# Performance work log

Hardware: AMD Instinct MI355X
Metric: run time of the kernel (lower is better)

## Reference

```python
import jax, jax.numpy as jnp
import numpy as np

N = 100000

def gcn_conv(x, src, dst, norm, W, b, num_nodes):
    # x: [N, Cin] -> [N, Cout]; GCNConv: linear transform then normalized sum aggregation
    h = x @ W                                   # [N, Cout]
    msg = h[src] * norm[:, None]                # [E+N, Cout] gather + scale
    out = jax.ops.segment_sum(msg, dst, num_segments=num_nodes)  # scatter-add
    return out + b

def _norm_coeffs(src, dst, num_nodes):
    # symmetric normalization D^{-1/2} A_hat D^{-1/2} with self-loops already in src/dst
    deg = jax.ops.segment_sum(jnp.ones_like(src, dtype=jnp.float32), dst, num_segments=num_nodes)
    dinv = jnp.where(deg > 0, jax.lax.rsqrt(jnp.maximum(deg, 1.0)), 0.0)
    return dinv[src] * dinv[dst]

def setup_inputs() -> dict:
    key = jax.random.key(0)
    ks = jax.random.split(key, 8)
    Cin, Ch, Cout, E = 128, 128, 47, 1600000
    x = jax.random.normal(ks[0], (N, Cin), dtype=jnp.float32)
    edge_index = jax.random.randint(ks[1], (2, E), 0, N, dtype=jnp.int64)
    def glorot(k, fan_in, fan_out):
        s = jnp.sqrt(6.0 / (fan_in + fan_out))
        return jax.random.uniform(k, (fan_in, fan_out), jnp.float32, -s, s)
    return {
        'x': x, 'edge_index': edge_index,
        'W1': glorot(ks[2], Cin, Ch), 'b1': jnp.zeros((Ch,), jnp.float32),
        'W2': glorot(ks[3], Ch, Ch),  'b2': jnp.zeros((Ch,), jnp.float32),
        'W3': glorot(ks[4], Ch, Cout),'b3': jnp.zeros((Cout,), jnp.float32),
    }

def reference(x, edge_index, W1, b1, W2, b2, W3, b3):
    num_nodes = x.shape[0]
    loop = jnp.arange(num_nodes, dtype=edge_index.dtype)
    src = jnp.concatenate([edge_index[0], loop])
    dst = jnp.concatenate([edge_index[1], loop])
    norm = _norm_coeffs(src, dst, num_nodes)
    # eval-mode forward: dropout(p=0.5, training=False) is identity
    h = gcn_conv(x, src, dst, norm, W1, b1, num_nodes)
    h = jax.nn.relu(h)
    h = gcn_conv(h, src, dst, norm, W2, b2, num_nodes)
    h = jax.nn.relu(h)
    h = gcn_conv(h, src, dst, norm, W3, b3, num_nodes)
    return jax.nn.log_softmax(h, axis=1)
```

## Files before the change

kernel.cpp:

```cpp
#include <hip/hip_runtime.h>
#include <stdint.h>

typedef __bf16 bf16x8 __attribute__((ext_vector_type(8)));
typedef float f32x4 __attribute__((ext_vector_type(4)));

#define CHB 8192

__device__ __forceinline__ float bf2f(unsigned short s) {
    union { unsigned u; float f; } x; x.u = ((unsigned)s) << 16; return x.f;
}
__device__ __forceinline__ float bitf(unsigned u) {
    union { unsigned u; float f; } x; x.u = u; return x.f;
}
__device__ __forceinline__ unsigned short f2bf(float f) {
    union { float f; unsigned u; } x; x.f = f;
    unsigned r = x.u + 0x7fffu + ((x.u >> 16) & 1u);
    return (unsigned short)(r >> 16);
}

__device__ __forceinline__ void dot2acc(float& a, unsigned pk, unsigned sel) {
    asm("v_dot2_f32_bf16 %0, %1, %2, %0" : "+v"(a) : "v"(pk), "v"(sel));
}

__global__ __launch_bounds__(256) void k_hist(const int* __restrict__ dst, int E, int nPB,
                                              int* __restrict__ bhist, int NB) {
    __shared__ int h[256];
    int t = threadIdx.x;
    h[t] = 0;
    __syncthreads();
    int blk = blockIdx.x;
    int hi = min((blk + 1) * CHB, E);
    for (int e = blk * CHB + t; e < hi; e += 256) atomicAdd(&h[dst[e] >> 9], 1);
    __syncthreads();
    if (t < NB) bhist[t * nPB + blk] = h[t];
}

__global__ __launch_bounds__(256) void k_scan_part(const int* __restrict__ deg,
                                                   int* __restrict__ part, int N) {
    __shared__ int wsum[4];
    int t = threadIdx.x;
    int lane = t & 63, wv = t >> 6;
    int base = blockIdx.x * 1024 + t * 4;
    int s = 0;
#pragma unroll
    for (int j = 0; j < 4; ++j) {
        int i = base + j;
        if (i < N) s += deg[i];
    }
    for (int off = 1; off < 64; off <<= 1) s += __shfl_xor(s, off, 64);
    if (lane == 0) wsum[wv] = s;
    __syncthreads();
    if (t == 0) part[blockIdx.x] = wsum[0] + wsum[1] + wsum[2] + wsum[3];
}

__global__ void k_scan_mid(int* __restrict__ part, int nb) {
    __shared__ int buf[256];
    int t = threadIdx.x;
    buf[t] = (t < nb) ? part[t] : 0;
    __syncthreads();
    for (int off = 1; off < 256; off <<= 1) {
        int v = buf[t];
        int u = (t >= off) ? buf[t - off] : 0;
        __syncthreads();
        buf[t] = v + u;
        __syncthreads();
    }
    if (t < nb) part[t] = (t == 0) ? 0 : buf[t - 1];
}

__global__ __launch_bounds__(256) void k_scan_final(const int* __restrict__ deg,
                                                    const int* __restrict__ part,
                                                    int* __restrict__ out, int N) {
    __shared__ int wsum[4];
    int t = threadIdx.x;
    int lane = t & 63, wv = t >> 6;
    int base = blockIdx.x * 1024 + t * 4;
    int v[4];
    int s = 0;
#pragma unroll
    for (int j = 0; j < 4; ++j) {
        int i = base + j;
        v[j] = (i < N) ? deg[i] : 0;
        s += v[j];
    }
    int inc = s;
    for (int off = 1; off < 64; off <<= 1) {
        int u = __shfl_up(inc, off, 64);
        if (lane >= off) inc += u;
    }
    if (lane == 63) wsum[wv] = inc;
    __syncthreads();
    int excl = part[blockIdx.x] + inc - s;
    for (int w = 0; w < wv; ++w) excl += wsum[w];
#pragma unroll
    for (int j = 0; j < 4; ++j) {
        int i = base + j;
        if (i < N) {
            out[i] = excl;
            excl += v[j];
            if (i == N - 1) out[N] = excl;
        }
    }
}

__global__ __launch_bounds__(256) void k_partition(const int* __restrict__ src,
                                                   const int* __restrict__ dst, int E,
                                                   int nPB, const int* __restrict__ bscan,
                                                   unsigned* __restrict__ part_edges, int NB) {
    __shared__ int cur[256];
    int t = threadIdx.x;
    int blk = blockIdx.x;
    if (t < NB) cur[t] = bscan[t * nPB + blk];
    __syncthreads();
    int hi = min((blk + 1) * CHB, E);
    for (int e = blk * CHB + t; e < hi; e += 256) {
        int d = dst[e];
        int s = src[e];
        int pos = atomicAdd(&cur[d >> 9], 1);
        part_edges[pos] = ((unsigned)(d & 511) << 17) | (unsigned)s;
    }
}

__global__ __launch_bounds__(256) void k_bucket(const unsigned* __restrict__ part_edges,
                                                const int* __restrict__ bscan, int nPB,
                                                int N, int Npad, int* __restrict__ row_ptr,
                                                float* __restrict__ dinv,
                                                int* __restrict__ ssrc) {
    __shared__ int cnt[512];
    __shared__ int excl[512];
    __shared__ int wsum[4];
    int t = threadIdx.x;
    int b = blockIdx.x;
    int pb = bscan[b * nPB];
    int pe = bscan[(b + 1) * nPB];
    cnt[t] = 0; cnt[t + 256] = 0;
    __syncthreads();
    for (int e = pb + t; e < pe; e += 256)
        atomicAdd(&cnt[(part_edges[e] >> 17) & 511], 1);
    __syncthreads();
    int a0 = cnt[2 * t], a1 = cnt[2 * t + 1];
    int s = a0 + a1;
    int lane = t & 63, wv = t >> 6;
    int inc = s;
    for (int off = 1; off < 64; off <<= 1) {
        int u = __shfl_up(inc, off, 64);
        if (lane >= off) inc += u;
    }
    if (lane == 63) wsum[wv] = inc;
    __syncthreads();
    int pre = inc - s;
    for (int w = 0; w < wv; ++w) pre += wsum[w];
    excl[2 * t] = pre;
    excl[2 * t + 1] = pre + a0;
    int base = b << 9;
#pragma unroll
    for (int j = 0; j < 2; ++j) {
        int i = 2 * t + j;
        int g = base + i;
        int c = (j == 0) ? a0 : a1;
        int ex = (j == 0) ? pre : pre + a0;
        if (g < N) {
            row_ptr[g] = pb + ex;
            if (g == N - 1) row_ptr[N] = pb + ex + c;
        }
        if (g < Npad) dinv[g] = rsqrtf((float)c + 1.0f);
    }
    __syncthreads();
    for (int e = pb + t; e < pe; e += 256) {
        unsigned pk = part_edges[e];
        int doff = (pk >> 17) & 511;
        int pos = pb + atomicAdd(&excl[doff], 1);
        ssrc[pos] = (int)(pk & 0x1FFFFu);
    }
}

__global__ void k_cvt_x(const float4* __restrict__ x, ushort4* __restrict__ out, int n4) {
    int i = blockIdx.x * blockDim.x + threadIdx.x;
    if (i < n4) {
        float4 v = x[i];
        ushort4 o;
        o.x = f2bf(v.x); o.y = f2bf(v.y); o.z = f2bf(v.z); o.w = f2bf(v.w);
        out[i] = o;
    }
}

__global__ void k_wfrag(const float* __restrict__ W, unsigned short* __restrict__ Wf,
                        int Ncol, int realCols) {
    int NT = Ncol >> 4;
    int total = 4 * NT * 64 * 8;
    int idx = blockIdx.x * blockDim.x + threadIdx.x;
    if (idx >= total) return;
    int j = idx & 7;
    int l = (idx >> 3) & 63;
    int t = idx >> 9;
    int n = t % NT;
    int kk = t / NT;
    int k = kk * 32 + ((l >> 4) << 3) + j;
    int c = (n << 4) + (l & 15);
    float v = (c < realCols) ? W[k * realCols + c] : 0.0f;
    Wf[idx] = f2bf(v);
}

template<int NT>
__global__ __launch_bounds__(256) void k_gemm(const unsigned short* __restrict__ A,
                                              const unsigned short* __restrict__ Wf,
                                              const float* __restrict__ dinv,
                                              unsigned short* __restrict__ Hout) {
    int lane = threadIdx.x & 63;
    int wv = threadIdx.x >> 6;
    int rb = blockIdx.x * 4 + wv;
    size_t row0 = (size_t)rb * 16;
    const unsigned short* arow = A + (row0 + (lane & 15)) * 128 + ((lane >> 4) << 3);
    f32x4 acc[NT];
#pragma unroll
    for (int n = 0; n < NT; ++n) acc[n] = (f32x4){0.f, 0.f, 0.f, 0.f};
#pragma unroll
    for (int kk = 0; kk < 4; ++kk) {
        bf16x8 a = *(const bf16x8*)(arow + kk * 32);
#pragma unroll
        for (int n = 0; n < NT; ++n) {
            bf16x8 b = *(const bf16x8*)(Wf + (((kk * NT + n) * 64 + lane) << 3));
            acc[n] = __builtin_amdgcn_mfma_f32_16x16x32_bf16(a, b, acc[n], 0, 0, 0);
        }
    }
    const int NCOL = NT * 16;
    size_t crow = row0 + ((lane >> 4) << 2);
    int ccol = lane & 15;
    float dv[4];
#pragma unroll
    for (int q = 0; q < 4; ++q) dv[q] = dinv[crow + q];
#pragma unroll
    for (int n = 0; n < NT; ++n) {
#pragma unroll
        for (int q = 0; q < 4; ++q) {
            Hout[(crow + q) * NCOL + n * 16 + ccol] = f2bf(acc[n][q] * dv[q]);
        }
    }
}

#define SEL_LO 0x00003F80u
#define SEL_HI 0x3F800000u

#define DOT8(v)                                      \
    dot2acc(acc[0], (v).x, sel_lo); dot2acc(acc[1], (v).x, sel_hi); \
    dot2acc(acc[2], (v).y, sel_lo); dot2acc(acc[3], (v).y, sel_hi); \
    dot2acc(acc[4], (v).z, sel_lo); dot2acc(acc[5], (v).z, sel_hi); \
    dot2acc(acc[6], (v).w, sel_lo); dot2acc(acc[7], (v).w, sel_hi);

#define DOT4(v)                                      \
    dot2acc(acc[0], (v).x, sel_lo); dot2acc(acc[1], (v).x, sel_hi); \
    dot2acc(acc[2], (v).y, sel_lo); dot2acc(acc[3], (v).y, sel_hi);

__global__ __launch_bounds__(256) void k_agg(const unsigned short* __restrict__ H,
                                             const int* __restrict__ row_ptr,
                                             const int* __restrict__ ssrc,
                                             const float* __restrict__ dinv,
                                             const float* __restrict__ bias,
                                             unsigned short* __restrict__ Out, int N) {
    int lane = threadIdx.x & 63;
    int i = blockIdx.x * 4 + (threadIdx.x >> 6);
    if (i >= N) return;
    unsigned sel_lo = SEL_LO, sel_hi = SEL_HI;
    int g = lane >> 4;
    int c16 = lane & 15;
    const uint4* Hv = (const uint4*)H;
    float acc[8];
#pragma unroll
    for (int c = 0; c < 8; ++c) acc[c] = 0.f;
    int e0 = row_ptr[i], e1 = row_ptr[i + 1];
    for (int base = e0; base < e1; base += 64) {
        int cnt = min(64, e1 - base);
        int sidx = (lane < cnt) ? ssrc[base + lane] : 0;
        int full = cnt & ~3;
#pragma unroll 4
        for (int j = 0; j < full; j += 4) {
            int s = __shfl(sidx, j + g, 64);
            uint4 v = Hv[((size_t)s << 4) + c16];
            DOT8(v);
        }
        int jj = full + g;
        if (jj < cnt) {
            int s = __shfl(sidx, jj, 64);
            uint4 v = Hv[((size_t)s << 4) + c16];
            DOT8(v);
        }
    }
    if (g == 0) {
        uint4 v = Hv[((size_t)i << 4) + c16];
        DOT8(v);
    }
#pragma unroll
    for (int c = 0; c < 8; ++c) {
        acc[c] += __shfl_xor(acc[c], 16, 64);
        acc[c] += __shfl_xor(acc[c], 32, 64);
    }
    if (g == 0) {
        float dv = dinv[i];
        const float4* bv = (const float4*)bias;
        float4 b0 = bv[c16 * 2], b1 = bv[c16 * 2 + 1];
        float r0 = fmaxf(acc[0] * dv + b0.x, 0.f);
        float r1 = fmaxf(acc[1] * dv + b0.y, 0.f);
        float r2 = fmaxf(acc[2] * dv + b0.z, 0.f);
        float r3 = fmaxf(acc[3] * dv + b0.w, 0.f);
        float r4 = fmaxf(acc[4] * dv + b1.x, 0.f);
        float r5 = fmaxf(acc[5] * dv + b1.y, 0.f);
        float r6 = fmaxf(acc[6] * dv + b1.z, 0.f);
        float r7 = fmaxf(acc[7] * dv + b1.w, 0.f);
        uint4 o;
        o.x = (unsigned)f2bf(r0) | ((unsigned)f2bf(r1) << 16);
        o.y = (unsigned)f2bf(r2) | ((unsigned)f2bf(r3) << 16);
        o.z = (unsigned)f2bf(r4) | ((unsigned)f2bf(r5) << 16);
        o.w = (unsigned)f2bf(r6) | ((unsigned)f2bf(r7) << 16);
        ((uint4*)Out)[((size_t)i << 4) + c16] = o;
    }
}

__global__ __launch_bounds__(256) void k_agg3(const unsigned short* __restrict__ H,
                                              const int* __restrict__ row_ptr,
                                              const int* __restrict__ ssrc,
                                              const float* __restrict__ dinv,
                                              const float* __restrict__ b3,
                                              float* __restrict__ Out, int N, int Cout) {
    int lane = threadIdx.x & 63;
    int i = blockIdx.x * 4 + (threadIdx.x >> 6);
    if (i >= N) return;
    unsigned sel_lo = SEL_LO, sel_hi = SEL_HI;
    int g = lane >> 4;
    int c16 = lane & 15;
    const uint2* Hv = (const uint2*)H;
    float acc[4];
#pragma unroll
    for (int c = 0; c < 4; ++c) acc[c] = 0.f;
    int e0 = row_ptr[i], e1 = row_ptr[i + 1];
    for (int base = e0; base < e1; base += 64) {
        int cnt = min(64, e1 - base);
        int sidx = (lane < cnt) ? ssrc[base + lane] : 0;
        int full = cnt & ~3;
#pragma unroll 4
        for (int j = 0; j < full; j += 4) {
            int s = __shfl(sidx, j + g, 64);
            uint2 v = Hv[((size_t)s << 4) + c16];
            DOT4(v);
        }
        int jj = full + g;
        if (jj < cnt) {
            int s = __shfl(sidx, jj, 64);
            uint2 v = Hv[((size_t)s << 4) + c16];
            DOT4(v);
        }
    }
    if (g == 0) {
        uint2 v = Hv[((size_t)i << 4) + c16];
        DOT4(v);
    }
#pragma unroll
    for (int c = 0; c < 4; ++c) {
        acc[c] += __shfl_xor(acc[c], 16, 64);
        acc[c] += __shfl_xor(acc[c], 32, 64);
    }
    float t0 = __shfl(acc[0], lane >> 2, 64);
    float t1 = __shfl(acc[1], lane >> 2, 64);
    float t2 = __shfl(acc[2], lane >> 2, 64);
    float t3 = __shfl(acc[3], lane >> 2, 64);
    float a01 = (lane & 1) ? t1 : t0;
    float a23 = (lane & 1) ? t3 : t2;
    float av  = (lane & 2) ? a23 : a01;
    float dv = dinv[i];
    float z = (lane < Cout) ? av * dv + b3[lane] : -1e30f;
    float m = z;
    for (int off = 32; off; off >>= 1) m = fmaxf(m, __shfl_xor(m, off, 64));
    float pexp = (lane < Cout) ? expf(z - m) : 0.f;
    float ssum = pexp;
    for (int off = 32; off; off >>= 1) ssum += __shfl_xor(ssum, off, 64);
    if (lane < Cout) Out[(size_t)i * Cout + lane] = z - m - logf(ssum);
}

extern "C" void kernel_launch(void* const* d_in, const int* in_sizes, int n_in,
                              void* d_out, int out_size, void* d_ws, size_t ws_size,
                              hipStream_t stream) {
    const float* x  = (const float*)d_in[0];
    const int*   ei = (const int*)d_in[1];
    const float* W1 = (const float*)d_in[2];
    const float* b1 = (const float*)d_in[3];
    const float* W2 = (const float*)d_in[4];
    const float* b2 = (const float*)d_in[5];
    const float* W3 = (const float*)d_in[6];
    const float* b3 = (const float*)d_in[7];

    const int N = in_sizes[0] / 128;
    const int E = in_sizes[1] / 2;
    const int Cout = in_sizes[7];
    const int Npad = (N + 63) & ~63;
    const int* srcp = ei;
    const int* dstp = ei + E;

    const int NB  = (N + 511) >> 9;
    const int nPB = (E + CHB - 1) / CHB;
    const int M   = NB * nPB;

    char* p = (char*)d_ws;
    auto alloc = [&](size_t bytes) -> void* {
        void* r = (void*)p;
        p += (bytes + 255) & ~(size_t)255;
        return r;
    };
    float* dinv     = (float*)alloc((size_t)Npad * 4);
    int*   row_ptr  = (int*)alloc((size_t)(N + 1) * 4);
    int*   bhist    = (int*)alloc((size_t)M * 4);
    int*   bscan    = (int*)alloc((size_t)(M + 1) * 4);
    int*   part     = (int*)alloc(1024 * 4);
    unsigned* pedge = (unsigned*)alloc((size_t)E * 4);
    int*   ssrc     = (int*)alloc((size_t)E * 4);
    unsigned short* xb  = (unsigned short*)alloc((size_t)Npad * 128 * 2);
    unsigned short* hb  = (unsigned short*)alloc((size_t)Npad * 128 * 2);
    unsigned short* ab  = (unsigned short*)alloc((size_t)Npad * 128 * 2);
    unsigned short* wf1 = (unsigned short*)alloc(128 * 128 * 2);
    unsigned short* wf2 = (unsigned short*)alloc(128 * 128 * 2);
    unsigned short* wf3 = (unsigned short*)alloc(128 * 64 * 2);

    const int nb2 = (M + 1023) / 1024;
    k_hist<<<nPB, 256, 0, stream>>>(dstp, E, nPB, bhist, NB);
    k_scan_part<<<nb2, 256, 0, stream>>>(bhist, part, M);
    k_scan_mid<<<1, 256, 0, stream>>>(part, nb2);
    k_scan_final<<<nb2, 256, 0, stream>>>(bhist, part, bscan, M);
    k_partition<<<nPB, 256, 0, stream>>>(srcp, dstp, E, nPB, bscan, pedge, NB);
    k_bucket<<<NB, 256, 0, stream>>>(pedge, bscan, nPB, N, Npad, row_ptr, dinv, ssrc);

    k_cvt_x<<<(N * 128 / 4 + 255) / 256, 256, 0, stream>>>((const float4*)x, (ushort4*)xb,
                                                           N * 128 / 4);
    k_wfrag<<<(16384 + 255) / 256, 256, 0, stream>>>(W1, wf1, 128, 128);
    k_wfrag<<<(16384 + 255) / 256, 256, 0, stream>>>(W2, wf2, 128, 128);
    k_wfrag<<<(8192 + 255) / 256, 256, 0, stream>>>(W3, wf3, 64, Cout);

    const int gemmGrid = Npad / 64;
    const int aggGrid = (N + 3) / 4;

    k_gemm<8><<<gemmGrid, 256, 0, stream>>>(xb, wf1, dinv, hb);
    k_agg<<<aggGrid, 256, 0, stream>>>(hb, row_ptr, ssrc, dinv, b1, ab, N);
    k_gemm<8><<<gemmGrid, 256, 0, stream>>>(ab, wf2, dinv, hb);
    k_agg<<<aggGrid, 256, 0, stream>>>(hb, row_ptr, ssrc, dinv, b2, ab, N);
    k_gemm<4><<<gemmGrid, 256, 0, stream>>>(ab, wf3, dinv, hb);
    k_agg3<<<aggGrid, 256, 0, stream>>>(hb, row_ptr, ssrc, dinv, b3,
                                        (float*)d_out, N, Cout);
}
```

Baseline: 303.7 us.

## Map one node per 16-lane quarter-wave in aggregation kernels

The aggregation kernels now assign each node to a 16-lane group instead of a full 64-lane wave, so each wave processes four nodes and every block covers sixteen. Each group walks its own edge list serially, loading indices directly, which removes the cross-group shuffles and the final reduction across lanes. The log-softmax in the last layer becomes a 16-lane reduction over four channels per lane. In exchange, lanes within a wave can diverge when neighbouring nodes have different degrees, and per-edge index loads are no longer coalesced.

```diff
diff --git a/kernel.cpp b/kernel.cpp
--- a/kernel.cpp
+++ b/kernel.cpp
@@ -8,9 +8,6 @@
 
 __device__ __forceinline__ float bf2f(unsigned short s) {
     union { unsigned u; float f; } x; x.u = ((unsigned)s) << 16; return x.f;
-}
-__device__ __forceinline__ float bitf(unsigned u) {
-    union { unsigned u; float f; } x; x.u = u; return x.f;
 }
 __device__ __forceinline__ unsigned short f2bf(float f) {
     union { float f; unsigned u; } x; x.f = f;
@@ -258,61 +255,43 @@
                                              const float* __restrict__ bias,
                                              unsigned short* __restrict__ Out, int N) {
     int lane = threadIdx.x & 63;
-    int i = blockIdx.x * 4 + (threadIdx.x >> 6);
+    int g = lane >> 4;
+    int c16 = lane & 15;
+    int i = blockIdx.x * 16 + ((threadIdx.x >> 6) << 2) + g;
     if (i >= N) return;
     unsigned sel_lo = SEL_LO, sel_hi = SEL_HI;
-    int g = lane >> 4;
-    int c16 = lane & 15;
     const uint4* Hv = (const uint4*)H;
     float acc[8];
 #pragma unroll
     for (int c = 0; c < 8; ++c) acc[c] = 0.f;
-    int e0 = row_ptr[i], e1 = row_ptr[i + 1];
-    for (int base = e0; base < e1; base += 64) {
-        int cnt = min(64, e1 - base);
-        int sidx = (lane < cnt) ? ssrc[base + lane] : 0;
-        int full = cnt & ~3;
-#pragma unroll 4
-        for (int j = 0; j < full; j += 4) {
-            int s = __shfl(sidx, j + g, 64);
-            uint4 v = Hv[((size_t)s << 4) + c16];
-            DOT8(v);
-        }
-        int jj = full + g;
-        if (jj < cnt) {
-            int s = __shfl(sidx, jj, 64);
-            uint4 v = Hv[((size_t)s << 4) + c16];
-            DOT8(v);
-        }
-    }
-    if (g == 0) {
+    {
         uint4 v = Hv[((size_t)i << 4) + c16];
         DOT8(v);
     }
-#pragma unroll
-    for (int c = 0; c < 8; ++c) {
-        acc[c] += __shfl_xor(acc[c], 16, 64);
-        acc[c] += __shfl_xor(acc[c], 32, 64);
-    }
-    if (g == 0) {
-        float dv = dinv[i];
-        const float4* bv = (const float4*)bias;
-        float4 b0 = bv[c16 * 2], b1 = bv[c16 * 2 + 1];
-        float r0 = fmaxf(acc[0] * dv + b0.x, 0.f);
-        float r1 = fmaxf(acc[1] * dv + b0.y, 0.f);
-        float r2 = fmaxf(acc[2] * dv + b0.z, 0.f);
-        float r3 = fmaxf(acc[3] * dv + b0.w, 0.f);
-        float r4 = fmaxf(acc[4] * dv + b1.x, 0.f);
-        float r5 = fmaxf(acc[5] * dv + b1.y, 0.f);
-        float r6 = fmaxf(acc[6] * dv + b1.z, 0.f);
-        float r7 = fmaxf(acc[7] * dv + b1.w, 0.f);
-        uint4 o;
-        o.x = (unsigned)f2bf(r0) | ((unsigned)f2bf(r1) << 16);
-        o.y = (unsigned)f2bf(r2) | ((unsigned)f2bf(r3) << 16);
-        o.z = (unsigned)f2bf(r4) | ((unsigned)f2bf(r5) << 16);
-        o.w = (unsigned)f2bf(r6) | ((unsigned)f2bf(r7) << 16);
-        ((uint4*)Out)[((size_t)i << 4) + c16] = o;
-    }
+    int e0 = row_ptr[i], e1 = row_ptr[i + 1];
+#pragma unroll 2
+    for (int e = e0; e < e1; ++e) {
+        int s = ssrc[e];
+        uint4 v = Hv[((size_t)s << 4) + c16];
+        DOT8(v);
+    }
+    float dv = dinv[i];
+    const float4* bv = (const float4*)bias;
+    float4 b0 = bv[c16 * 2], b1 = bv[c16 * 2 + 1];
+    float r0 = fmaxf(acc[0] * dv + b0.x, 0.f);
+    float r1 = fmaxf(acc[1] * dv + b0.y, 0.f);
+    float r2 = fmaxf(acc[2] * dv + b0.z, 0.f);
+    float r3 = fmaxf(acc[3] * dv + b0.w, 0.f);
+    float r4 = fmaxf(acc[4] * dv + b1.x, 0.f);
+    float r5 = fmaxf(acc[5] * dv + b1.y, 0.f);
+    float r6 = fmaxf(acc[6] * dv + b1.z, 0.f);
+    float r7 = fmaxf(acc[7] * dv + b1.w, 0.f);
+    uint4 o;
+    o.x = (unsigned)f2bf(r0) | ((unsigned)f2bf(r1) << 16);
+    o.y = (unsigned)f2bf(r2) | ((unsigned)f2bf(r3) << 16);
+    o.z = (unsigned)f2bf(r4) | ((unsigned)f2bf(r5) << 16);
+    o.w = (unsigned)f2bf(r6) | ((unsigned)f2bf(r7) << 16);
+    ((uint4*)Out)[((size_t)i << 4) + c16] = o;
 }
 
 __global__ __launch_bounds__(256) void k_agg3(const unsigned short* __restrict__ H,
@@ -322,57 +301,51 @@
                                               const float* __restrict__ b3,
                                               float* __restrict__ Out, int N, int Cout) {
     int lane = threadIdx.x & 63;
-    int i = blockIdx.x * 4 + (threadIdx.x >> 6);
+    int g = lane >> 4;
+    int c16 = lane & 15;
+    int i = blockIdx.x * 16 + ((threadIdx.x >> 6) << 2) + g;
     if (i >= N) return;
     unsigned sel_lo = SEL_LO, sel_hi = SEL_HI;
-    int g = lane >> 4;
-    int c16 = lane & 15;
     const uint2* Hv = (const uint2*)H;
     float acc[4];
 #pragma unroll
     for (int c = 0; c < 4; ++c) acc[c] = 0.f;
-    int e0 = row_ptr[i], e1 = row_ptr[i + 1];
-    for (int base = e0; base < e1; base += 64) {
-        int cnt = min(64, e1 - base);
-        int sidx = (lane < cnt) ? ssrc[base + lane] : 0;
-        int full = cnt & ~3;
-#pragma unroll 4
-        for (int j = 0; j < full; j += 4) {
-            int s = __shfl(sidx, j + g, 64);
-            uint2 v = Hv[((size_t)s << 4) + c16];
-            DOT4(v);
-        }
-        int jj = full + g;
-        if (jj < cnt) {
-            int s = __shfl(sidx, jj, 64);
-            uint2 v = Hv[((size_t)s << 4) + c16];
-            DOT4(v);
-        }
-    }
-    if (g == 0) {
+    {
         uint2 v = Hv[((size_t)i << 4) + c16];
         DOT4(v);
     }
+    int e0 = row_ptr[i], e1 = row_ptr[i + 1];
+#pragma unroll 2
+    for (int e = e0; e < e1; ++e) {
+        int s = ssrc[e];
+        uint2 v = Hv[((size_t)s << 4) + c16];
+        DOT4(v);
+    }
+    float dv = dinv[i];
+    float z[4];
+    float m = -1e30f;
 #pragma unroll
     for (int c = 0; c < 4; ++c) {
-        acc[c] += __shfl_xor(acc[c], 16, 64);
-        acc[c] += __shfl_xor(acc[c], 32, 64);
-    }
-    float t0 = __shfl(acc[0], lane >> 2, 64);
-    float t1 = __shfl(acc[1], lane >> 2, 64);
-    float t2 = __shfl(acc[2], lane >> 2, 64);
-    float t3 = __shfl(acc[3], lane >> 2, 64);
-    float a01 = (lane & 1) ? t1 : t0;
-    float a23 = (lane & 1) ? t3 : t2;
-    float av  = (lane & 2) ? a23 : a01;
-    float dv = dinv[i];
-    float z = (lane < Cout) ? av * dv + b3[lane] : -1e30f;
-    float m = z;
-    for (int off = 32; off; off >>= 1) m = fmaxf(m, __shfl_xor(m, off, 64));
-    float pexp = (lane < Cout) ? expf(z - m) : 0.f;
-    float ssum = pexp;
-    for (int off = 32; off; off >>= 1) ssum += __shfl_xor(ssum, off, 64);
-    if (lane < Cout) Out[(size_t)i * Cout + lane] = z - m - logf(ssum);
+        int ch = c16 * 4 + c;
+        z[c] = (ch < Cout) ? acc[c] * dv + b3[ch] : -1e30f;
+        m = fmaxf(m, z[c]);
+    }
+#pragma unroll
+    for (int off = 1; off < 16; off <<= 1) m = fmaxf(m, __shfl_xor(m, off, 64));
+    float ssum = 0.f;
+#pragma unroll
+    for (int c = 0; c < 4; ++c) {
+        int ch = c16 * 4 + c;
+        if (ch < Cout) ssum += expf(z[c] - m);
+    }
+#pragma unroll
+    for (int off = 1; off < 16; off <<= 1) ssum += __shfl_xor(ssum, off, 64);
+    float lg = m + logf(ssum);
+#pragma unroll
+    for (int c = 0; c < 4; ++c) {
+        int ch = c16 * 4 + c;
+        if (ch < Cout) Out[(size_t)i * Cout + ch] = z[c] - lg;
+    }
 }
 
 extern "C" void kernel_launch(void* const* d_in, const int* in_sizes, int n_in,
@@ -433,7 +406,7 @@
     k_wfrag<<<(8192 + 255) / 256, 256, 0, stream>>>(W3, wf3, 64, Cout);
 
     const int gemmGrid = Npad / 64;
-    const int aggGrid = (N + 3) / 4;
+    const int aggGrid = (N + 15) / 16;
 
     k_gemm<8><<<gemmGrid, 256, 0, stream>>>(xb, wf1, dinv, hb);
     k_agg<<<aggGrid, 256, 0, stream>>>(hb, row_ptr, ssrc, dinv, b1, ab, N);
```

New measurement: 322.1 us. 6.0% more time.

## Fuse aggregation with next-layer GEMM via LDS and fold x conversion into GEMM

Applied to the files above, without the earlier changes.

The first GEMM now reads fp32 x directly and converts to bf16 in registers, so the separate conversion kernel and its bf16 buffer go away. Each aggregation for layers 1 and 2 is fused with the following layer's MFMA GEMM. A block aggregates 64 nodes into an LDS tile, then multiplies that tile by the next weight matrix, which removes a full write and re-read of the intermediate activation. In exchange, each wave walks 16 nodes one after another, and there are far fewer blocks. That cuts the parallelism available to hide the latency of the irregular gathers and can leave load imbalance across waves.

```diff
diff --git a/kernel.cpp b/kernel.cpp
--- a/kernel.cpp
+++ b/kernel.cpp
@@ -5,13 +5,8 @@
 typedef float f32x4 __attribute__((ext_vector_type(4)));
 
 #define CHB 8192
-
-__device__ __forceinline__ float bf2f(unsigned short s) {
-    union { unsigned u; float f; } x; x.u = ((unsigned)s) << 16; return x.f;
-}
-__device__ __forceinline__ float bitf(unsigned u) {
-    union { unsigned u; float f; } x; x.u = u; return x.f;
-}
+#define LDSROW 17
+
 __device__ __forceinline__ unsigned short f2bf(float f) {
     union { float f; unsigned u; } x; x.f = f;
     unsigned r = x.u + 0x7fffu + ((x.u >> 16) & 1u);
@@ -21,6 +16,19 @@
 __device__ __forceinline__ void dot2acc(float& a, unsigned pk, unsigned sel) {
     asm("v_dot2_f32_bf16 %0, %1, %2, %0" : "+v"(a) : "v"(pk), "v"(sel));
 }
+
+#define SEL_LO 0x00003F80u
+#define SEL_HI 0x3F800000u
+
+#define DOT8(v)                                      \
+    dot2acc(acc[0], (v).x, sel_lo); dot2acc(acc[1], (v).x, sel_hi); \
+    dot2acc(acc[2], (v).y, sel_lo); dot2acc(acc[3], (v).y, sel_hi); \
+    dot2acc(acc[4], (v).z, sel_lo); dot2acc(acc[5], (v).z, sel_hi); \
+    dot2acc(acc[6], (v).w, sel_lo); dot2acc(acc[7], (v).w, sel_hi);
+
+#define DOT4(v)                                      \
+    dot2acc(acc[0], (v).x, sel_lo); dot2acc(acc[1], (v).x, sel_hi); \
+    dot2acc(acc[2], (v).y, sel_lo); dot2acc(acc[3], (v).y, sel_hi);
 
 __global__ __launch_bounds__(256) void k_hist(const int* __restrict__ dst, int E, int nPB,
                                               int* __restrict__ bhist, int NB) {
@@ -171,16 +179,6 @@
         int doff = (pk >> 17) & 511;
         int pos = pb + atomicAdd(&excl[doff], 1);
         ssrc[pos] = (int)(pk & 0x1FFFFu);
-    }
-}
-
-__global__ void k_cvt_x(const float4* __restrict__ x, ushort4* __restrict__ out, int n4) {
-    int i = blockIdx.x * blockDim.x + threadIdx.x;
-    if (i < n4) {
-        float4 v = x[i];
-        ushort4 o;
-        o.x = f2bf(v.x); o.y = f2bf(v.y); o.z = f2bf(v.z); o.w = f2bf(v.w);
-        out[i] = o;
     }
 }
 
@@ -201,117 +199,153 @@
     Wf[idx] = f2bf(v);
 }
 
-template<int NT>
-__global__ __launch_bounds__(256) void k_gemm(const unsigned short* __restrict__ A,
-                                              const unsigned short* __restrict__ Wf,
-                                              const float* __restrict__ dinv,
-                                              unsigned short* __restrict__ Hout) {
+__global__ __launch_bounds__(256) void k_gemm_f32(const float* __restrict__ X,
+                                                  const unsigned short* __restrict__ Wf,
+                                                  const float* __restrict__ dinv,
+                                                  unsigned short* __restrict__ Hout, int N) {
     int lane = threadIdx.x & 63;
     int wv = threadIdx.x >> 6;
-    int rb = blockIdx.x * 4 + wv;
-    size_t row0 = (size_t)rb * 16;
-    const unsigned short* arow = A + (row0 + (lane & 15)) * 128 + ((lane >> 4) << 3);
-    f32x4 acc[NT];
-#pragma unroll
-    for (int n = 0; n < NT; ++n) acc[n] = (f32x4){0.f, 0.f, 0.f, 0.f};
+    size_t row0 = (size_t)(blockIdx.x * 4 + wv) * 16;
+    int arowi = (int)row0 + (lane & 15);
+    const float* arow = X + (size_t)arowi * 128 + ((lane >> 4) << 3);
+    bool vr = arowi < N;
+    f32x4 acc[8];
+#pragma unroll
+    for (int n = 0; n < 8; ++n) acc[n] = (f32x4){0.f, 0.f, 0.f, 0.f};
 #pragma unroll
     for (int kk = 0; kk < 4; ++kk) {
-        bf16x8 a = *(const bf16x8*)(arow + kk * 32);
-#pragma unroll
-        for (int n = 0; n < NT; ++n) {
-            bf16x8 b = *(const bf16x8*)(Wf + (((kk * NT + n) * 64 + lane) << 3));
-            acc[n] = __builtin_amdgcn_mfma_f32_16x16x32_bf16(a, b, acc[n], 0, 0, 0);
-        }
-    }
-    const int NCOL = NT * 16;
+        union { bf16x8 v; unsigned short u[8]; } A;
+        if (vr) {
+            float4 f0 = *(const float4*)(arow + kk * 32);
+            float4 f1 = *(const float4*)(arow + kk * 32 + 4);
+            A.u[0] = f2bf(f0.x); A.u[1] = f2bf(f0.y);
+            A.u[2] = f2bf(f0.z); A.u[3] = f2bf(f0.w);
+            A.u[4] = f2bf(f1.x); A.u[5] = f2bf(f1.y);
+            A.u[6] = f2bf(f1.z); A.u[7] = f2bf(f1.w);
+        } else {
+#pragma unroll
+            for (int j = 0; j < 8; ++j) A.u[j] = 0;
+        }
+#pragma unroll
+        for (int n = 0; n < 8; ++n) {
+            bf16x8 b = *(const bf16x8*)(Wf + (((kk * 8 + n) * 64 + lane) << 3));
+            acc[n] = __builtin_amdgcn_mfma_f32_16x16x32_bf16(A.v, b, acc[n], 0, 0, 0);
+        }
+    }
     size_t crow = row0 + ((lane >> 4) << 2);
     int ccol = lane & 15;
     float dv[4];
 #pragma unroll
     for (int q = 0; q < 4; ++q) dv[q] = dinv[crow + q];
 #pragma unroll
-    for (int n = 0; n < NT; ++n) {
+    for (int n = 0; n < 8; ++n) {
 #pragma unroll
         for (int q = 0; q < 4; ++q) {
-            Hout[(crow + q) * NCOL + n * 16 + ccol] = f2bf(acc[n][q] * dv[q]);
-        }
-    }
-}
-
-#define SEL_LO 0x00003F80u
-#define SEL_HI 0x3F800000u
-
-#define DOT8(v)                                      \
-    dot2acc(acc[0], (v).x, sel_lo); dot2acc(acc[1], (v).x, sel_hi); \
-    dot2acc(acc[2], (v).y, sel_lo); dot2acc(acc[3], (v).y, sel_hi); \
-    dot2acc(acc[4], (v).z, sel_lo); dot2acc(acc[5], (v).z, sel_hi); \
-    dot2acc(acc[6], (v).w, sel_lo); dot2acc(acc[7], (v).w, sel_hi);
-
-#define DOT4(v)                                      \
-    dot2acc(acc[0], (v).x, sel_lo); dot2acc(acc[1], (v).x, sel_hi); \
-    dot2acc(acc[2], (v).y, sel_lo); dot2acc(acc[3], (v).y, sel_hi);
-
-__global__ __launch_bounds__(256) void k_agg(const unsigned short* __restrict__ H,
-                                             const int* __restrict__ row_ptr,
-                                             const int* __restrict__ ssrc,
-                                             const float* __restrict__ dinv,
-                                             const float* __restrict__ bias,
-                                             unsigned short* __restrict__ Out, int N) {
+            Hout[(crow + q) * 128 + n * 16 + ccol] = f2bf(acc[n][q] * dv[q]);
+        }
+    }
+}
+
+template<int NT>
+__global__ __launch_bounds__(256) void k_agg_gemm(const unsigned short* __restrict__ H,
+                                                  const int* __restrict__ row_ptr,
+                                                  const int* __restrict__ ssrc,
+                                                  const float* __restrict__ dinv,
+                                                  const float* __restrict__ bias,
+                                                  const unsigned short* __restrict__ Wf,
+                                                  unsigned short* __restrict__ Hout, int N) {
+    __shared__ uint4 lds[64 * LDSROW];
     int lane = threadIdx.x & 63;
-    int i = blockIdx.x * 4 + (threadIdx.x >> 6);
-    if (i >= N) return;
-    unsigned sel_lo = SEL_LO, sel_hi = SEL_HI;
+    int wv = threadIdx.x >> 6;
     int g = lane >> 4;
     int c16 = lane & 15;
+    unsigned sel_lo = SEL_LO, sel_hi = SEL_HI;
     const uint4* Hv = (const uint4*)H;
-    float acc[8];
-#pragma unroll
-    for (int c = 0; c < 8; ++c) acc[c] = 0.f;
-    int e0 = row_ptr[i], e1 = row_ptr[i + 1];
-    for (int base = e0; base < e1; base += 64) {
-        int cnt = min(64, e1 - base);
-        int sidx = (lane < cnt) ? ssrc[base + lane] : 0;
-        int full = cnt & ~3;
+    const int iBase = blockIdx.x * 64 + wv * 16;
+
+    for (int ii = 0; ii < 16; ++ii) {
+        int i = iBase + ii;
+        float acc[8];
+#pragma unroll
+        for (int c = 0; c < 8; ++c) acc[c] = 0.f;
+        if (i < N) {
+            if (g == 0) {
+                uint4 v = Hv[((size_t)i << 4) + c16];
+                DOT8(v);
+            }
+            int e0 = row_ptr[i], e1 = row_ptr[i + 1];
+            for (int base = e0; base < e1; base += 64) {
+                int cnt = min(64, e1 - base);
+                int sidx = (lane < cnt) ? ssrc[base + lane] : 0;
+                int full = cnt & ~3;
 #pragma unroll 4
-        for (int j = 0; j < full; j += 4) {
-            int s = __shfl(sidx, j + g, 64);
-            uint4 v = Hv[((size_t)s << 4) + c16];
-            DOT8(v);
-        }
-        int jj = full + g;
-        if (jj < cnt) {
-            int s = __shfl(sidx, jj, 64);
-            uint4 v = Hv[((size_t)s << 4) + c16];
-            DOT8(v);
-        }
-    }
-    if (g == 0) {
-        uint4 v = Hv[((size_t)i << 4) + c16];
-        DOT8(v);
-    }
-#pragma unroll
-    for (int c = 0; c < 8; ++c) {
-        acc[c] += __shfl_xor(acc[c], 16, 64);
-        acc[c] += __shfl_xor(acc[c], 32, 64);
-    }
-    if (g == 0) {
-        float dv = dinv[i];
-        const float4* bv = (const float4*)bias;
-        float4 b0 = bv[c16 * 2], b1 = bv[c16 * 2 + 1];
-        float r0 = fmaxf(acc[0] * dv + b0.x, 0.f);
-        float r1 = fmaxf(acc[1] * dv + b0.y, 0.f);
-        float r2 = fmaxf(acc[2] * dv + b0.z, 0.f);
-        float r3 = fmaxf(acc[3] * dv + b0.w, 0.f);
-        float r4 = fmaxf(acc[4] * dv + b1.x, 0.f);
-        float r5 = fmaxf(acc[5] * dv + b1.y, 0.f);
-        float r6 = fmaxf(acc[6] * dv + b1.z, 0.f);
-        float r7 = fmaxf(acc[7] * dv + b1.w, 0.f);
-        uint4 o;
-        o.x = (unsigned)f2bf(r0) | ((unsigned)f2bf(r1) << 16);
-        o.y = (unsigned)f2bf(r2) | ((unsigned)f2bf(r3) << 16);
-        o.z = (unsigned)f2bf(r4) | ((unsigned)f2bf(r5) << 16);
-        o.w = (unsigned)f2bf(r6) | ((unsigned)f2bf(r7) << 16);
-        ((uint4*)Out)[((size_t)i << 4) + c16] = o;
+                for (int j = 0; j < full; j += 4) {
+                    int s = __shfl(sidx, j + g, 64);
+                    uint4 v = Hv[((size_t)s << 4) + c16];
+                    DOT8(v);
+                }
+                int jj = full + g;
+                if (jj < cnt) {
+                    int s = __shfl(sidx, jj, 64);
+                    uint4 v = Hv[((size_t)s << 4) + c16];
+                    DOT8(v);
+                }
+            }
+        }
+#pragma unroll
+        for (int c = 0; c < 8; ++c) {
+            acc[c] += __shfl_xor(acc[c], 16, 64);
+            acc[c] += __shfl_xor(acc[c], 32, 64);
+        }
+        if (g == 0) {
+            float dv = dinv[i];
+            const float4* bv = (const float4*)bias;
+            float4 b0 = bv[c16 * 2], b1 = bv[c16 * 2 + 1];
+            float r0 = fmaxf(acc[0] * dv + b0.x, 0.f);
+            float r1 = fmaxf(acc[1] * dv + b0.y, 0.f);
+            float r2 = fmaxf(acc[2] * dv + b0.z, 0.f);
+            float r3 = fmaxf(acc[3] * dv + b0.w, 0.f);
+            float r4 = fmaxf(acc[4] * dv + b1.x, 0.f);
+            float r5 = fmaxf(acc[5] * dv + b1.y, 0.f);
+            float r6 = fmaxf(acc[6] * dv + b1.z, 0.f);
+            float r7 = fmaxf(acc[7] * dv + b1.w, 0.f);
+            uint4 o;
+            o.x = (unsigned)f2bf(r0) | ((unsigned)f2bf(r1) << 16);
+            o.y = (unsigned)f2bf(r2) | ((unsigned)f2bf(r3) << 16);
+            o.z = (unsigned)f2bf(r4) | ((unsigned)f2bf(r5) << 16);
+            o.w = (unsigned)f2bf(r6) | ((unsigned)f2bf(r7) << 16);
+            lds[(wv * 16 + ii) * LDSROW + c16] = o;
+        }
+    }
+    __syncthreads();
+
+    f32x4 gacc[NT];
+#pragma unroll
+    for (int n = 0; n < NT; ++n) gacc[n] = (f32x4){0.f, 0.f, 0.f, 0.f};
+    const uint4* arow = &lds[(wv * 16 + (lane & 15)) * LDSROW];
+#pragma unroll
+    for (int kk = 0; kk < 4; ++kk) {
+        union { bf16x8 v; uint4 q; } A;
+        A.q = arow[kk * 4 + (lane >> 4)];
+#pragma unroll
+        for (int n = 0; n < NT; ++n) {
+            bf16x8 b = *(const bf16x8*)(Wf + (((kk * NT + n) * 64 + lane) << 3));
+            gacc[n] = __builtin_amdgcn_mfma_f32_16x16x32_bf16(A.v, b, gacc[n], 0, 0, 0);
+        }
+    }
+    const int NCOL = NT * 16;
+    size_t row0 = (size_t)iBase;
+    size_t crow = row0 + ((lane >> 4) << 2);
+    int ccol = lane & 15;
+    float dv[4];
+#pragma unroll
+    for (int q = 0; q < 4; ++q) dv[q] = dinv[crow + q];
+#pragma unroll
+    for (int n = 0; n < NT; ++n) {
+#pragma unroll
+        for (int q = 0; q < 4; ++q) {
+            Hout[(crow + q) * NCOL + n * 16 + ccol] = f2bf(gacc[n][q] * dv[q]);
+        }
     }
 }
 
@@ -411,7 +445,6 @@
     int*   part     = (int*)alloc(1024 * 4);
     unsigned* pedge = (unsigned*)alloc((size_t)E * 4);
     int*   ssrc     = (int*)alloc((size_t)E * 4);
-    unsigned short* xb  = (unsigned short*)alloc((size_t)Npad * 128 * 2);
     unsigned short* hb  = (unsigned short*)alloc((size_t)Npad * 128 * 2);
     unsigned short* ab  = (unsigned short*)alloc((size_t)Npad * 128 * 2);
     unsigned short* wf1 = (unsigned short*)alloc(128 * 128 * 2);
@@ -426,8 +459,6 @@
     k_partition<<<nPB, 256, 0, stream>>>(srcp, dstp, E, nPB, bscan, pedge, NB);
     k_bucket<<<NB, 256, 0, stream>>>(pedge, bscan, nPB, N, Npad, row_ptr, dinv, ssrc);
 
-    k_cvt_x<<<(N * 128 / 4 + 255) / 256, 256, 0, stream>>>((const float4*)x, (ushort4*)xb,
-                                                           N * 128 / 4);
     k_wfrag<<<(16384 + 255) / 256, 256, 0, stream>>>(W1, wf1, 128, 128);
     k_wfrag<<<(16384 + 255) / 256, 256, 0, stream>>>(W2, wf2, 128, 128);
     k_wfrag<<<(8192 + 255) / 256, 256, 0, stream>>>(W3, wf3, 64, Cout);
@@ -435,11 +466,9 @@
     const int gemmGrid = Npad / 64;
     const int aggGrid = (N + 3) / 4;
 
-    k_gemm<8><<<gemmGrid, 256, 0, stream>>>(xb, wf1, dinv, hb);
-    k_agg<<<aggGrid, 256, 0, stream>>>(hb, row_ptr, ssrc, dinv, b1, ab, N);
-    k_gemm<8><<<gemmGrid, 256, 0, stream>>>(ab, wf2, dinv, hb);
-    k_agg<<<aggGrid, 256, 0, stream>>>(hb, row_ptr, ssrc, dinv, b2, ab, N);
-    k_gemm<4><<<gemmGrid, 256, 0, stream>>>(ab, wf3, dinv, hb);
+    k_gemm_f32<<<gemmGrid, 256, 0, stream>>>(x, wf1, dinv, hb, N);
+    k_agg_gemm<8><<<gemmGrid, 256, 0, stream>>>(hb, row_ptr, ssrc, dinv, b1, wf2, ab, N);
+    k_agg_gemm<4><<<gemmGrid, 256, 0, stream>>>(ab, row_ptr, ssrc, dinv, b2, wf3, hb, N);
     k_agg3<<<aggGrid, 256, 0, stream>>>(hb, row_ptr, ssrc, dinv, b3,
                                         (float*)d_out, N, Cout);
 }
```

Measured after the change: 324.9 us. 1.07x slower.
